# Performance work log

Measured on AMD Instinct MI355X. Metric: run time of the kernel, lower is better.

## Reference

```python
import jax, jax.numpy as jnp
import numpy as np

EPS = 1e-5
QB = 127.0  # 2**(8-1) - 1


def absmean_quantize(w):
    """Ternary quantization (BitNet b1.58): gamma = mean|W|, W_q in {-1,0,1}."""
    gamma = jnp.mean(jnp.abs(w))
    u = w / jnp.maximum(gamma, EPS)
    w_q = jnp.clip(jnp.round(u), -1.0, 1.0)
    return w_q, gamma


def absmax_quantize(x, bits=8):
    """Per-token int8 absmax quantization: alpha = max|x| over last dim."""
    qb = float(2 ** (bits - 1) - 1)
    alpha = jnp.max(jnp.abs(x), axis=-1, keepdims=True)  # [..., 1]
    u = x * qb / jnp.maximum(alpha, EPS)
    x_q = jnp.clip(jnp.round(u), -qb, qb)
    return x_q, alpha


def setup_inputs() -> dict:
    key = jax.random.key(0)
    k1, k2 = jax.random.split(key)
    B, S, D_IN, D_OUT = 4, 2048, 2048, 8192
    x = jax.random.normal(k1, (B, S, D_IN), dtype=jnp.float32)
    # kaiming-uniform-ish init scale for weight [out, in]
    bound = 1.0 / np.sqrt(D_IN)
    weight = jax.random.uniform(k2, (D_OUT, D_IN), minval=-bound, maxval=bound, dtype=jnp.float32)
    return {"x": x, "weight": weight}


def reference(x, weight):
    w_q, gamma = absmean_quantize(weight)          # [O,I], scalar
    x_q, alpha = absmax_quantize(x, bits=8)        # [B,S,I], [B,S,1]
    out = jnp.einsum('bsi,oi->bso', x_q, w_q)      # float matmul of quantized values
    scale = alpha * gamma / QB                     # [B,S,1]
    return out * scale
```

## Files before the change

kernel.cpp:

```cpp
#include <hip/hip_runtime.h>
#include <hip/hip_bf16.h>
#include <stdint.h>

typedef unsigned short u16;
typedef int i32x4 __attribute__((ext_vector_type(4)));

#define K_DIM 2048
#define M_DIM 8192
#define N_DIM 8192
#define QBF   127.0f
#define EPSF  1e-5f
#define NT    32

__device__ __forceinline__ void load_lds16(const void* gsrc, void* ldst) {
    __builtin_amdgcn_global_load_lds(
        (__attribute__((address_space(1))) void*)gsrc,
        (__attribute__((address_space(3))) void*)ldst,
        16, 0, 0);
}

__global__ __launch_bounds__(256) void k_abs_partial(const float* __restrict__ w,
                                                     float* __restrict__ partial) {
    __shared__ float red[256];
    int t = threadIdx.x, b = blockIdx.x;
    const float4* w4 = (const float4*)w;
    size_t base = (size_t)b * 2048;
    float s = 0.f;
#pragma unroll
    for (int j = 0; j < 8; ++j) {
        float4 v = w4[base + j * 256 + t];
        s += fabsf(v.x) + fabsf(v.y) + fabsf(v.z) + fabsf(v.w);
    }
    red[t] = s; __syncthreads();
    for (int off = 128; off > 0; off >>= 1) {
        if (t < off) red[t] += red[t + off];
        __syncthreads();
    }
    if (t == 0) partial[b] = red[0];
}

__global__ __launch_bounds__(256) void k_gamma(const float* __restrict__ partial,
                                               float* __restrict__ gamma) {
    __shared__ float red[256];
    int t = threadIdx.x;
    float s = 0.f;
#pragma unroll
    for (int j = 0; j < 8; ++j) s += partial[t + j * 256];
    red[t] = s; __syncthreads();
    for (int off = 128; off > 0; off >>= 1) {
        if (t < off) red[t] += red[t + off];
        __syncthreads();
    }
    if (t == 0) gamma[0] = red[0] / 16777216.0f;
}

__global__ __launch_bounds__(256) void k_quant_w(const float* __restrict__ w,
                                                 const float* __restrict__ gamma,
                                                 uint* __restrict__ wq) {
    float g = fmaxf(gamma[0], EPSF);
    int tid = blockIdx.x * 256 + threadIdx.x;
    float4 v = ((const float4*)w)[tid];
    int a = (int)fminf(fmaxf(rintf(v.x / g), -1.f), 1.f);
    int b = (int)fminf(fmaxf(rintf(v.y / g), -1.f), 1.f);
    int c = (int)fminf(fmaxf(rintf(v.z / g), -1.f), 1.f);
    int d = (int)fminf(fmaxf(rintf(v.w / g), -1.f), 1.f);
    wq[tid] = (a & 255) | ((b & 255) << 8) | ((c & 255) << 16) | ((d & 255) << 24);
}

__global__ __launch_bounds__(256) void k_quant_x(const float* __restrict__ x,
                                                 uint* __restrict__ xq,
                                                 float* __restrict__ alpha) {
    __shared__ float red[256];
    int t = threadIdx.x, row = blockIdx.x;
    const float4* x4 = (const float4*)x + (size_t)row * 512;
    float4 v0 = x4[t], v1 = x4[t + 256];
    float m = fmaxf(fmaxf(fabsf(v0.x), fabsf(v0.y)), fmaxf(fabsf(v0.z), fabsf(v0.w)));
    m = fmaxf(m, fmaxf(fmaxf(fabsf(v1.x), fabsf(v1.y)), fmaxf(fabsf(v1.z), fabsf(v1.w))));
    red[t] = m; __syncthreads();
    for (int off = 128; off > 0; off >>= 1) {
        if (t < off) red[t] = fmaxf(red[t], red[t + off]);
        __syncthreads();
    }
    float a = red[0];
    if (t == 0) alpha[row] = a;
    float den = fmaxf(a, EPSF);
    uint* q = xq + (size_t)row * 512;
    int q0 = (int)fminf(fmaxf(rintf(v0.x * QBF / den), -QBF), QBF);
    int q1 = (int)fminf(fmaxf(rintf(v0.y * QBF / den), -QBF), QBF);
    int q2 = (int)fminf(fmaxf(rintf(v0.z * QBF / den), -QBF), QBF);
    int q3 = (int)fminf(fmaxf(rintf(v0.w * QBF / den), -QBF), QBF);
    q[t] = (q0 & 255) | ((q1 & 255) << 8) | ((q2 & 255) << 16) | ((q3 & 255) << 24);
    q0 = (int)fminf(fmaxf(rintf(v1.x * QBF / den), -QBF), QBF);
    q1 = (int)fminf(fmaxf(rintf(v1.y * QBF / den), -QBF), QBF);
    q2 = (int)fminf(fmaxf(rintf(v1.z * QBF / den), -QBF), QBF);
    q3 = (int)fminf(fmaxf(rintf(v1.w * QBF / den), -QBF), QBF);
    q[t + 256] = (q0 & 255) | ((q1 & 255) << 8) | ((q2 & 255) << 16) | ((q3 & 255) << 24);
}

__global__ __launch_bounds__(512, 2) void k_gemm(const uint8_t* __restrict__ xq,
                                                 const uint8_t* __restrict__ wq,
                                                 const float* __restrict__ alpha,
                                                 const float* __restrict__ gamma,
                                                 float* __restrict__ out) {
    __shared__ __align__(16) char smem[131072];

    int bid = blockIdx.x;
    int wg = (bid & 7) * 128 + (bid >> 3);
    int tm = wg >> 5, tn = wg & 31;

    int t = threadIdx.x;
    int w = t >> 6, l = t & 63;
    int wr = w >> 2, wc = w & 3;

    const uint8_t* srcb[4];
    int dstq[4];
    {
        int rsub = l >> 2;
        int clog = (l & 3) ^ ((rsub >> 1) & 3);
#pragma unroll
        for (int j = 0; j < 4; ++j) {
            int q = w * 4 + j;
            int isB = q >> 4;
            int r = (q & 15) * 16 + rsub;
            int grow = (isB ? tn : tm) * 256 + r;
            srcb[j] = (isB ? wq : xq) + (size_t)grow * K_DIM + clog * 16;
            dstq[j] = q * 1024;
        }
    }

    i32x4 acc[8][4];
#pragma unroll
    for (int m = 0; m < 8; ++m)
#pragma unroll
        for (int n = 0; n < 4; ++n) acc[m][n] = (i32x4){0, 0, 0, 0};

    int lrow = l & 15, kgrp = l >> 4;
    int cph = (kgrp ^ ((lrow >> 1) & 3)) * 16;
    int aoff = (wr * 128 + lrow) * 64 + cph;
    int boff = 16384 + (wc * 64 + lrow) * 64 + cph;

#pragma unroll
    for (int p = 0; p < 3; ++p)
#pragma unroll
        for (int j = 0; j < 4; ++j)
            load_lds16(srcb[j] + (size_t)p * 64, smem + p * 32768 + dstq[j]);

    for (int kt = 0; kt < NT; ++kt) {
        char* sb = smem + (kt & 3) * 32768;
        if (kt < NT - 2)       asm volatile("s_waitcnt vmcnt(8)" ::: "memory");
        else if (kt == NT - 2) asm volatile("s_waitcnt vmcnt(4)" ::: "memory");
        else                   asm volatile("s_waitcnt vmcnt(0)" ::: "memory");
        __builtin_amdgcn_s_barrier();

        i32x4 a[8], b[4];
#pragma unroll
        for (int i = 0; i < 4; ++i)
            b[i] = *(const i32x4*)(sb + boff + i * 1024);
#pragma unroll
        for (int i = 0; i < 4; ++i)
            a[i] = *(const i32x4*)(sb + aoff + i * 1024);
        if (kt + 3 < NT) {
            char* db = smem + ((kt + 3) & 3) * 32768;
#pragma unroll
            for (int j = 0; j < 4; ++j)
                load_lds16(srcb[j] + (size_t)(kt + 3) * 64, db + dstq[j]);
        }
#pragma unroll
        for (int i = 4; i < 8; ++i)
            a[i] = *(const i32x4*)(sb + aoff + i * 1024);

        asm volatile("s_waitcnt lgkmcnt(4)" ::: "memory");
        __builtin_amdgcn_sched_barrier(0);
        __builtin_amdgcn_s_setprio(1);
#pragma unroll
        for (int m = 0; m < 4; ++m)
#pragma unroll
            for (int n = 0; n < 4; ++n)
                acc[m][n] = __builtin_amdgcn_mfma_i32_16x16x64_i8(
                    a[m], b[n], acc[m][n], 0, 0, 0);
        __builtin_amdgcn_s_setprio(0);

        asm volatile("s_waitcnt lgkmcnt(0)" ::: "memory");
        __builtin_amdgcn_sched_barrier(0);
        __builtin_amdgcn_s_setprio(1);
#pragma unroll
        for (int m = 0; m < 4; ++m)
#pragma unroll
            for (int n = 0; n < 4; ++n)
                acc[m + 4][n] = __builtin_amdgcn_mfma_i32_16x16x64_i8(
                    a[m + 4], b[n], acc[m + 4][n], 0, 0, 0);
        __builtin_amdgcn_s_setprio(0);
    }

    float gam = gamma[0];
    int orow0 = tm * 256 + wr * 128 + kgrp * 4;
    int ocol = tn * 256 + wc * 64 + lrow;
#pragma unroll
    for (int mf = 0; mf < 8; ++mf)
#pragma unroll
        for (int r = 0; r < 4; ++r) {
            int row = orow0 + mf * 16 + r;
            float s = alpha[row] * gam / QBF;
            size_t rb = (size_t)row * N_DIM + ocol;
#pragma unroll
            for (int nf = 0; nf < 4; ++nf)
                out[rb + nf * 16] = (float)acc[mf][nf][r] * s;
        }
}

extern "C" void kernel_launch(void* const* d_in, const int* in_sizes, int n_in,
                              void* d_out, int out_size, void* d_ws, size_t ws_size,
                              hipStream_t stream) {
    const float* x  = (const float*)d_in[0];
    const float* wt = (const float*)d_in[1];
    float* out = (float*)d_out;

    char* ws = (char*)d_ws;
    uint8_t* xq     = (uint8_t*)ws;
    uint8_t* wq     = (uint8_t*)(ws + 16777216);
    float* alpha    = (float*)(ws + 33554432);
    float* partial  = (float*)(ws + 33587200);
    float* gamma    = (float*)(ws + 33595392);

    k_abs_partial<<<2048, 256, 0, stream>>>(wt, partial);
    k_gamma<<<1, 256, 0, stream>>>(partial, gamma);
    k_quant_w<<<16384, 256, 0, stream>>>(wt, gamma, (uint*)wq);
    k_quant_x<<<8192, 256, 0, stream>>>(x, (uint*)xq, alpha);
    k_gemm<<<1024, 512, 0, stream>>>(xq, wq, alpha, gamma, out);
}
```

Measured before the change: 216.1 us.

## Shrink GEMM tile to 128x128 with 32x32x32 int8 MFMA and smaller K step

The int8 GEMM moves from 256x256 tiles with 8 waves, a 64-wide K step and 16x16x64 MFMAs to 128x128 tiles with 4 waves, a 32-wide K step and 32x32x32 MFMAs. LDS per block drops from 128KB to 32KB, so more blocks can be resident per CU and more tiles are launched. The 4-stage async global-to-LDS pipeline stays, but the XOR swizzle is gone. In exchange, each loaded byte is reused less, global traffic goes up, and there are twice as many K iterations, each with a barrier.

```diff
diff --git a/kernel.cpp b/kernel.cpp
--- a/kernel.cpp
+++ b/kernel.cpp
@@ -2,15 +2,15 @@
 #include <hip/hip_bf16.h>
 #include <stdint.h>
 
-typedef unsigned short u16;
 typedef int i32x4 __attribute__((ext_vector_type(4)));
+typedef int i32x16 __attribute__((ext_vector_type(16)));
 
 #define K_DIM 2048
 #define M_DIM 8192
 #define N_DIM 8192
 #define QBF   127.0f
 #define EPSF  1e-5f
-#define NT    32
+#define NT    64
 
 __device__ __forceinline__ void load_lds16(const void* gsrc, void* ldst) {
     __builtin_amdgcn_global_load_lds(
@@ -97,115 +97,94 @@
     q[t + 256] = (q0 & 255) | ((q1 & 255) << 8) | ((q2 & 255) << 16) | ((q3 & 255) << 24);
 }
 
-__global__ __launch_bounds__(512, 2) void k_gemm(const uint8_t* __restrict__ xq,
+__global__ __launch_bounds__(256, 4) void k_gemm(const uint8_t* __restrict__ xq,
                                                  const uint8_t* __restrict__ wq,
                                                  const float* __restrict__ alpha,
                                                  const float* __restrict__ gamma,
                                                  float* __restrict__ out) {
-    __shared__ __align__(16) char smem[131072];
+    __shared__ __align__(16) char smem[32768];
 
     int bid = blockIdx.x;
-    int wg = (bid & 7) * 128 + (bid >> 3);
-    int tm = wg >> 5, tn = wg & 31;
+    int wg = (bid & 7) * 512 + (bid >> 3);
+    int tm = wg >> 6, tn = wg & 63;
 
     int t = threadIdx.x;
     int w = t >> 6, l = t & 63;
-    int wr = w >> 2, wc = w & 3;
-
-    const uint8_t* srcb[4];
-    int dstq[4];
-    {
-        int rsub = l >> 2;
-        int clog = (l & 3) ^ ((rsub >> 1) & 3);
-#pragma unroll
-        for (int j = 0; j < 4; ++j) {
-            int q = w * 4 + j;
-            int isB = q >> 4;
-            int r = (q & 15) * 16 + rsub;
-            int grow = (isB ? tn : tm) * 256 + r;
-            srcb[j] = (isB ? wq : xq) + (size_t)grow * K_DIM + clog * 16;
-            dstq[j] = q * 1024;
-        }
-    }
-
-    i32x4 acc[8][4];
-#pragma unroll
-    for (int m = 0; m < 8; ++m)
-#pragma unroll
-        for (int n = 0; n < 4; ++n) acc[m][n] = (i32x4){0, 0, 0, 0};
-
-    int lrow = l & 15, kgrp = l >> 4;
-    int cph = (kgrp ^ ((lrow >> 1) & 3)) * 16;
-    int aoff = (wr * 128 + lrow) * 64 + cph;
-    int boff = 16384 + (wc * 64 + lrow) * 64 + cph;
+    int wr = w >> 1, wc = w & 1;
+
+    const uint8_t* srcb[2];
+    int dstq[2];
+#pragma unroll
+    for (int j = 0; j < 2; ++j) {
+        int fj = w * 2 + j;
+        int isB = fj >> 2;
+        int fi = fj & 3;
+        int row = fi * 32 + (l & 31);
+        int kc = l >> 5;
+        int grow = (isB ? tn : tm) * 128 + row;
+        srcb[j] = (isB ? wq : xq) + (size_t)grow * K_DIM + kc * 16;
+        dstq[j] = fj * 1024;
+    }
+
+    i32x16 acc[2][2];
+#pragma unroll
+    for (int m = 0; m < 2; ++m)
+#pragma unroll
+        for (int n = 0; n < 2; ++n) acc[m][n] = (i32x16){0};
+
+    int aoff[2], boff[2];
+#pragma unroll
+    for (int i = 0; i < 2; ++i) {
+        aoff[i] = (wr * 2 + i) * 1024 + l * 16;
+        boff[i] = 4096 + (wc * 2 + i) * 1024 + l * 16;
+    }
 
 #pragma unroll
     for (int p = 0; p < 3; ++p)
 #pragma unroll
-        for (int j = 0; j < 4; ++j)
-            load_lds16(srcb[j] + (size_t)p * 64, smem + p * 32768 + dstq[j]);
+        for (int j = 0; j < 2; ++j)
+            load_lds16(srcb[j] + (size_t)p * 32, smem + p * 8192 + dstq[j]);
 
     for (int kt = 0; kt < NT; ++kt) {
-        char* sb = smem + (kt & 3) * 32768;
-        if (kt < NT - 2)       asm volatile("s_waitcnt vmcnt(8)" ::: "memory");
-        else if (kt == NT - 2) asm volatile("s_waitcnt vmcnt(4)" ::: "memory");
+        char* sb = smem + (kt & 3) * 8192;
+        if (kt < NT - 2)       asm volatile("s_waitcnt vmcnt(4)" ::: "memory");
+        else if (kt == NT - 2) asm volatile("s_waitcnt vmcnt(2)" ::: "memory");
         else                   asm volatile("s_waitcnt vmcnt(0)" ::: "memory");
         __builtin_amdgcn_s_barrier();
 
-        i32x4 a[8], b[4];
-#pragma unroll
-        for (int i = 0; i < 4; ++i)
-            b[i] = *(const i32x4*)(sb + boff + i * 1024);
-#pragma unroll
-        for (int i = 0; i < 4; ++i)
-            a[i] = *(const i32x4*)(sb + aoff + i * 1024);
+        i32x4 a0 = *(const i32x4*)(sb + aoff[0]);
+        i32x4 a1 = *(const i32x4*)(sb + aoff[1]);
+        i32x4 b0 = *(const i32x4*)(sb + boff[0]);
+        i32x4 b1 = *(const i32x4*)(sb + boff[1]);
         if (kt + 3 < NT) {
-            char* db = smem + ((kt + 3) & 3) * 32768;
-#pragma unroll
-            for (int j = 0; j < 4; ++j)
-                load_lds16(srcb[j] + (size_t)(kt + 3) * 64, db + dstq[j]);
+            char* db = smem + ((kt + 3) & 3) * 8192;
+            load_lds16(srcb[0] + (size_t)(kt + 3) * 32, db + dstq[0]);
+            load_lds16(srcb[1] + (size_t)(kt + 3) * 32, db + dstq[1]);
         }
-#pragma unroll
-        for (int i = 4; i < 8; ++i)
-            a[i] = *(const i32x4*)(sb + aoff + i * 1024);
-
-        asm volatile("s_waitcnt lgkmcnt(4)" ::: "memory");
-        __builtin_amdgcn_sched_barrier(0);
-        __builtin_amdgcn_s_setprio(1);
-#pragma unroll
-        for (int m = 0; m < 4; ++m)
-#pragma unroll
-            for (int n = 0; n < 4; ++n)
-                acc[m][n] = __builtin_amdgcn_mfma_i32_16x16x64_i8(
-                    a[m], b[n], acc[m][n], 0, 0, 0);
-        __builtin_amdgcn_s_setprio(0);
-
         asm volatile("s_waitcnt lgkmcnt(0)" ::: "memory");
         __builtin_amdgcn_sched_barrier(0);
         __builtin_amdgcn_s_setprio(1);
-#pragma unroll
-        for (int m = 0; m < 4; ++m)
-#pragma unroll
-            for (int n = 0; n < 4; ++n)
-                acc[m + 4][n] = __builtin_amdgcn_mfma_i32_16x16x64_i8(
-                    a[m + 4], b[n], acc[m + 4][n], 0, 0, 0);
+        acc[0][0] = __builtin_amdgcn_mfma_i32_32x32x32_i8(a0, b0, acc[0][0], 0, 0, 0);
+        acc[0][1] = __builtin_amdgcn_mfma_i32_32x32x32_i8(a0, b1, acc[0][1], 0, 0, 0);
+        acc[1][0] = __builtin_amdgcn_mfma_i32_32x32x32_i8(a1, b0, acc[1][0], 0, 0, 0);
+        acc[1][1] = __builtin_amdgcn_mfma_i32_32x32x32_i8(a1, b1, acc[1][1], 0, 0, 0);
         __builtin_amdgcn_s_setprio(0);
     }
 
-    float gam = gamma[0];
-    int orow0 = tm * 256 + wr * 128 + kgrp * 4;
-    int ocol = tn * 256 + wc * 64 + lrow;
-#pragma unroll
-    for (int mf = 0; mf < 8; ++mf)
-#pragma unroll
-        for (int r = 0; r < 4; ++r) {
-            int row = orow0 + mf * 16 + r;
-            float s = alpha[row] * gam / QBF;
-            size_t rb = (size_t)row * N_DIM + ocol;
-#pragma unroll
-            for (int nf = 0; nf < 4; ++nf)
-                out[rb + nf * 16] = (float)acc[mf][nf][r] * s;
+    float gs = gamma[0] / QBF;
+    int hi = l >> 5, lc = l & 31;
+#pragma unroll
+    for (int mi = 0; mi < 2; ++mi) {
+        int rowb = tm * 128 + wr * 64 + mi * 32 + hi * 4;
+#pragma unroll
+        for (int reg = 0; reg < 16; ++reg) {
+            int row = rowb + (reg & 3) + 8 * (reg >> 2);
+            float s = alpha[row] * gs;
+            size_t rb = (size_t)row * N_DIM + tn * 128 + wc * 64 + lc;
+            out[rb]      = (float)acc[mi][0][reg] * s;
+            out[rb + 32] = (float)acc[mi][1][reg] * s;
         }
+    }
 }
 
 extern "C" void kernel_launch(void* const* d_in, const int* in_sizes, int n_in,
@@ -226,5 +205,5 @@
     k_gamma<<<1, 256, 0, stream>>>(partial, gamma);
     k_quant_w<<<16384, 256, 0, stream>>>(wt, gamma, (uint*)wq);
     k_quant_x<<<8192, 256, 0, stream>>>(x, (uint*)xq, alpha);
-    k_gemm<<<1024, 512, 0, stream>>>(xq, wq, alpha, gamma, out);
-}
+    k_gemm<<<4096, 256, 0, stream>>>(xq, wq, alpha, gamma, out);
+}
```

Measured after the change: 347.3 us. 1.61x slower.

## Shrink GEMM tile to 256x128 with 4 waves and 3-stage LDS ring

Applied to the files above, without the earlier changes.

Changes the int8 GEMM from 512-thread blocks computing 256x256 tiles to 256-thread blocks computing 256x128 tiles. The grid doubles to 2048 blocks, and the LDS ring buffer drops from 4 stages to 3 at 24 KB each, so two blocks can fit per CU. The aim is more resident blocks for latency hiding and better balance across CUs. The cost is lower operand reuse per block, since the x tile is re-read twice as often, plus a shallower prefetch depth.

```diff
diff --git a/kernel.cpp b/kernel.cpp
--- a/kernel.cpp
+++ b/kernel.cpp
@@ -2,7 +2,6 @@
 #include <hip/hip_bf16.h>
 #include <stdint.h>
 
-typedef unsigned short u16;
 typedef int i32x4 __attribute__((ext_vector_type(4)));
 
 #define K_DIM 2048
@@ -97,32 +96,32 @@
     q[t + 256] = (q0 & 255) | ((q1 & 255) << 8) | ((q2 & 255) << 16) | ((q3 & 255) << 24);
 }
 
-__global__ __launch_bounds__(512, 2) void k_gemm(const uint8_t* __restrict__ xq,
+__global__ __launch_bounds__(256, 2) void k_gemm(const uint8_t* __restrict__ xq,
                                                  const uint8_t* __restrict__ wq,
                                                  const float* __restrict__ alpha,
                                                  const float* __restrict__ gamma,
                                                  float* __restrict__ out) {
-    __shared__ __align__(16) char smem[131072];
+    __shared__ __align__(16) char smem[73728];
 
     int bid = blockIdx.x;
-    int wg = (bid & 7) * 128 + (bid >> 3);
-    int tm = wg >> 5, tn = wg & 31;
+    int wg = (bid & 7) * 256 + (bid >> 3);
+    int tm = wg >> 6, tn = wg & 63;
 
     int t = threadIdx.x;
     int w = t >> 6, l = t & 63;
-    int wr = w >> 2, wc = w & 3;
-
-    const uint8_t* srcb[4];
-    int dstq[4];
+    int wr = w >> 1, wc = w & 1;
+
+    const uint8_t* srcb[6];
+    int dstq[6];
     {
         int rsub = l >> 2;
         int clog = (l & 3) ^ ((rsub >> 1) & 3);
 #pragma unroll
-        for (int j = 0; j < 4; ++j) {
-            int q = w * 4 + j;
+        for (int j = 0; j < 6; ++j) {
+            int q = w * 6 + j;
             int isB = q >> 4;
-            int r = (q & 15) * 16 + rsub;
-            int grow = (isB ? tn : tm) * 256 + r;
+            int r = (isB ? (q & 7) : q) * 16 + rsub;
+            int grow = isB ? tn * 128 + r : tm * 256 + r;
             srcb[j] = (isB ? wq : xq) + (size_t)grow * K_DIM + clog * 16;
             dstq[j] = q * 1024;
         }
@@ -136,71 +135,76 @@
 
     int lrow = l & 15, kgrp = l >> 4;
     int cph = (kgrp ^ ((lrow >> 1) & 3)) * 16;
-    int aoff = (wr * 128 + lrow) * 64 + cph;
-    int boff = 16384 + (wc * 64 + lrow) * 64 + cph;
-
-#pragma unroll
-    for (int p = 0; p < 3; ++p)
-#pragma unroll
-        for (int j = 0; j < 4; ++j)
-            load_lds16(srcb[j] + (size_t)p * 64, smem + p * 32768 + dstq[j]);
-
+    int aoff[8], boff[4];
+#pragma unroll
+    for (int mf = 0; mf < 8; ++mf) aoff[mf] = (wr * 128 + mf * 16 + lrow) * 64 + cph;
+#pragma unroll
+    for (int nf = 0; nf < 4; ++nf) boff[nf] = 16384 + (wc * 64 + nf * 16 + lrow) * 64 + cph;
+
+#pragma unroll
+    for (int p = 0; p < 2; ++p)
+#pragma unroll
+        for (int j = 0; j < 6; ++j)
+            load_lds16(srcb[j] + (size_t)p * 64, smem + p * 24576 + dstq[j]);
+
+    int slot = 0;
     for (int kt = 0; kt < NT; ++kt) {
-        char* sb = smem + (kt & 3) * 32768;
-        if (kt < NT - 2)       asm volatile("s_waitcnt vmcnt(8)" ::: "memory");
-        else if (kt == NT - 2) asm volatile("s_waitcnt vmcnt(4)" ::: "memory");
-        else                   asm volatile("s_waitcnt vmcnt(0)" ::: "memory");
+        char* sb = smem + slot * 24576;
+        if (kt < NT - 1) asm volatile("s_waitcnt vmcnt(6)" ::: "memory");
+        else             asm volatile("s_waitcnt vmcnt(0)" ::: "memory");
         __builtin_amdgcn_s_barrier();
 
         i32x4 a[8], b[4];
 #pragma unroll
-        for (int i = 0; i < 4; ++i)
-            b[i] = *(const i32x4*)(sb + boff + i * 1024);
-#pragma unroll
-        for (int i = 0; i < 4; ++i)
-            a[i] = *(const i32x4*)(sb + aoff + i * 1024);
-        if (kt + 3 < NT) {
-            char* db = smem + ((kt + 3) & 3) * 32768;
-#pragma unroll
-            for (int j = 0; j < 4; ++j)
-                load_lds16(srcb[j] + (size_t)(kt + 3) * 64, db + dstq[j]);
+        for (int mf = 0; mf < 4; ++mf) a[mf] = *(const i32x4*)(sb + aoff[mf]);
+#pragma unroll
+        for (int nf = 0; nf < 4; ++nf) b[nf] = *(const i32x4*)(sb + boff[nf]);
+        __builtin_amdgcn_sched_barrier(0);
+        if (kt + 2 < NT) {
+            int ds = slot + 2; if (ds >= 3) ds -= 3;
+            char* db = smem + ds * 24576;
+#pragma unroll
+            for (int j = 0; j < 6; ++j)
+                load_lds16(srcb[j] + (size_t)(kt + 2) * 64, db + dstq[j]);
         }
-#pragma unroll
-        for (int i = 4; i < 8; ++i)
-            a[i] = *(const i32x4*)(sb + aoff + i * 1024);
+        __builtin_amdgcn_sched_barrier(0);
+#pragma unroll
+        for (int mf = 4; mf < 8; ++mf) a[mf] = *(const i32x4*)(sb + aoff[mf]);
 
         asm volatile("s_waitcnt lgkmcnt(4)" ::: "memory");
         __builtin_amdgcn_sched_barrier(0);
         __builtin_amdgcn_s_setprio(1);
 #pragma unroll
-        for (int m = 0; m < 4; ++m)
-#pragma unroll
-            for (int n = 0; n < 4; ++n)
-                acc[m][n] = __builtin_amdgcn_mfma_i32_16x16x64_i8(
-                    a[m], b[n], acc[m][n], 0, 0, 0);
+        for (int mf = 0; mf < 4; ++mf)
+#pragma unroll
+            for (int nf = 0; nf < 4; ++nf)
+                acc[mf][nf] = __builtin_amdgcn_mfma_i32_16x16x64_i8(
+                    a[mf], b[nf], acc[mf][nf], 0, 0, 0);
         __builtin_amdgcn_s_setprio(0);
 
         asm volatile("s_waitcnt lgkmcnt(0)" ::: "memory");
         __builtin_amdgcn_sched_barrier(0);
         __builtin_amdgcn_s_setprio(1);
 #pragma unroll
-        for (int m = 0; m < 4; ++m)
-#pragma unroll
-            for (int n = 0; n < 4; ++n)
-                acc[m + 4][n] = __builtin_amdgcn_mfma_i32_16x16x64_i8(
-                    a[m + 4], b[n], acc[m + 4][n], 0, 0, 0);
+        for (int mf = 4; mf < 8; ++mf)
+#pragma unroll
+            for (int nf = 0; nf < 4; ++nf)
+                acc[mf][nf] = __builtin_amdgcn_mfma_i32_16x16x64_i8(
+                    a[mf], b[nf], acc[mf][nf], 0, 0, 0);
         __builtin_amdgcn_s_setprio(0);
-    }
-
-    float gam = gamma[0];
+
+        slot = (slot == 2) ? 0 : slot + 1;
+    }
+
+    float gs = gamma[0] / QBF;
     int orow0 = tm * 256 + wr * 128 + kgrp * 4;
-    int ocol = tn * 256 + wc * 64 + lrow;
+    int ocol = tn * 128 + wc * 64 + lrow;
 #pragma unroll
     for (int mf = 0; mf < 8; ++mf)
 #pragma unroll
         for (int r = 0; r < 4; ++r) {
             int row = orow0 + mf * 16 + r;
-            float s = alpha[row] * gam / QBF;
+            float s = alpha[row] * gs;
             size_t rb = (size_t)row * N_DIM + ocol;
 #pragma unroll
             for (int nf = 0; nf < 4; ++nf)
@@ -226,5 +230,5 @@
     k_gamma<<<1, 256, 0, stream>>>(partial, gamma);
     k_quant_w<<<16384, 256, 0, stream>>>(wt, gamma, (uint*)wq);
     k_quant_x<<<8192, 256, 0, stream>>>(x, (uint*)xq, alpha);
-    k_gemm<<<1024, 512, 0, stream>>>(xq, wq, alpha, gamma, out);
-}
+    k_gemm<<<2048, 256, 0, stream>>>(xq, wq, alpha, gamma, out);
+}
```

Result: slower. 222.1 us (+2.8%).
